# Optimization experiments

Measured on AMD Instinct MI355X. Metric: run time of the kernel, lower is better.

Reference implementation:

```python
import jax, jax.numpy as jnp
import numpy as np

DEPTH_K = 64
DEPTH_V = 64
NUM_HEADS = 8


def setup_inputs() -> dict:
    key = jax.random.key(0)
    k1, k2, k3 = jax.random.split(key, 3)
    B, H, W = 2, 48, 48
    C = 2 * DEPTH_K + DEPTH_V  # 192
    dkh = DEPTH_K // NUM_HEADS  # 8
    inputs = jax.random.normal(k1, (B, H, W, C), dtype=jnp.float32)
    # RandomNormal(stddev=dkh**-0.5) initializer
    key_rel_w = jax.random.normal(k2, (2 * W - 1, dkh), dtype=jnp.float32) * dkh ** (-0.5)
    key_rel_h = jax.random.normal(k3, (2 * H - 1, dkh), dtype=jnp.float32) * dkh ** (-0.5)
    return {"inputs": inputs, "key_rel_w": key_rel_w, "key_rel_h": key_rel_h}


def rel_to_abs(x):
    # x: [B, N, L, 2L-1] -> [B, N, L, L] via the pad/reshape skew trick
    B, N, L, _ = x.shape
    x = jnp.pad(x, ((0, 0), (0, 0), (0, 0), (0, 1)))          # [B,N,L,2L]
    flat = x.reshape(B, N, L * 2 * L)
    flat = jnp.pad(flat, ((0, 0), (0, 0), (0, L - 1)))
    final = flat.reshape(B, N, L + 1, 2 * L - 1)
    return final[:, :, :L, L - 1:]


def rel_logits_1d(q, rel_k, transpose_mask):
    # q: [B, nh, H, W, d]; rel_k: [2W-1, d]
    B, nh, H, W, d = q.shape
    rl = jnp.einsum('bhxyd,md->bhxym', q, rel_k)              # [B,nh,H,W,2W-1]
    rl = rel_to_abs(rl.reshape(B, nh * H, W, 2 * W - 1))      # [B,nh*H,W,W]
    rl = rl.reshape(B, nh, H, W, W)
    rl = jnp.broadcast_to(rl[:, :, :, None, :, :], (B, nh, H, H, W, W))
    rl = jnp.transpose(rl, transpose_mask)
    return rl.reshape(B, nh, H * W, H * W)


def attention_augmentation_2d(inputs, key_rel_w, key_rel_h):
    B, H, W, C = inputs.shape
    nh = NUM_HEADS
    dkh = DEPTH_K // nh
    dvh = DEPTH_V // nh
    q, k, v = jnp.split(inputs, [DEPTH_K, 2 * DEPTH_K], axis=-1)

    def split_heads(x):
        d = x.shape[-1] // nh
        return jnp.transpose(x.reshape(B, H, W, nh, d), (0, 3, 1, 2, 4))  # [B,nh,H,W,d]

    q = split_heads(q) * dkh ** (-0.5)
    k = split_heads(k)
    v = split_heads(v)

    flat_q = q.reshape(B, nh, H * W, dkh)
    flat_k = k.reshape(B, nh, H * W, dkh)
    flat_v = v.reshape(B, nh, H * W, dvh)

    logits = jnp.einsum('bhnd,bhmd->bhnm', flat_q, flat_k)    # [B,nh,HW,HW]
    # relative logits: width uses q as-is, height uses q with H/W swapped
    w_rel = rel_logits_1d(q, key_rel_w, (0, 1, 2, 4, 3, 5))
    h_rel = rel_logits_1d(jnp.transpose(q, (0, 1, 3, 2, 4)), key_rel_h, (0, 1, 4, 2, 5, 3))
    logits = logits + h_rel + w_rel

    weights = jax.nn.softmax(logits, axis=-1)
    attn = jnp.einsum('bhnm,bhmd->bhnd', weights, flat_v)     # [B,nh,HW,dvh]
    attn = attn.reshape(B, nh, H, W, dvh)
    out = jnp.transpose(attn, (0, 2, 3, 1, 4)).reshape(B, H, W, DEPTH_V)
    return out


def reference(inputs, key_rel_w, key_rel_h):
    return attention_augmentation_2d(inputs, key_rel_w, key_rel_h)
```

## Files before the change

### kernel.cpp

```cpp
#include <hip/hip_runtime.h>
#include <stdint.h>

#define WW 48
#define NQ 2304
#define NWT 144
#define SCL 0.51011868f
#define SHIFT 17.312340491f
#define ACCF (NWT * 2304)

typedef float v2f __attribute__((ext_vector_type(2)));

__device__ __forceinline__ v2f v2fma(v2f a, v2f b, v2f c) {
    return __builtin_elementwise_fma(a, b, c);
}

__global__ __launch_bounds__(256) void qh_pre(const float* __restrict__ in,
                                              const float* __restrict__ relh,
                                              float* __restrict__ QH) {
    const int bh = blockIdx.x / 9;
    const int nt = blockIdx.x - bh * 9;
    const int n = nt * 256 + threadIdx.x;
    const int b = bh >> 3, h = bh & 7;
    const int y = n / WW;

    const float* qp = in + ((size_t)(b * NQ + n) * 192 + h * 8);
    float4 a = *(const float4*)qp, bb = *(const float4*)(qp + 4);
    v2f Q0 = {a.x * SCL, a.y * SCL}, Q1 = {a.z * SCL, a.w * SCL};
    v2f Q2 = {bb.x * SCL, bb.y * SCL}, Q3 = {bb.z * SCL, bb.w * SCL};

    for (int y2 = 0; y2 < 48; ++y2) {
        const float* rh = relh + (y2 - y + 47) * 8;
        float4 ta = *(const float4*)rh, tb = *(const float4*)(rh + 4);
        v2f s = v2fma(Q0, (v2f){ta.x, ta.y},
                v2fma(Q1, (v2f){ta.z, ta.w},
                v2fma(Q2, (v2f){tb.x, tb.y},
                      Q3 * (v2f){tb.z, tb.w})));
        QH[(size_t)(bh * 48 + y2) * 2304 + n] = s.x + s.y - SHIFT;
    }
}

__global__ __launch_bounds__(256, 2) void attn_kernel(const float* __restrict__ in,
                                                      const float* __restrict__ relw,
                                                      const float* __restrict__ QH,
                                                      float* __restrict__ ACC) {
    __shared__ float4 lds[1152];

    const int bx = blockIdx.x;
    const int wt = bx % NWT;
    const int gg = bx / NWT;
    const int bh = wt / 9;
    const int qt = wt - bh * 9;
    const int tid = threadIdx.x;
    const int lane = tid & 63;
    const int wv = tid >> 6;
    const int kc_local = wv >> 1;
    const int rowhalf = wv & 1;
    const int kc = gg * 2 + kc_local;
    const int b = bh >> 3, h = bh & 7;

    const float4* inp4 = (const float4*)in;
    for (int t = tid; t < 1152; t += 256) {
        const int chunk = t / 576, tt = t - chunk * 576;
        const int key = tt >> 2, p = tt & 3;
        const int row = key / 3, col = key - row * 3;
        const size_t px = (size_t)(b * NQ + row * 48 + (gg * 2 + chunk) * 3 + col) * 48;
        const int c4 = (p < 2) ? (16 + h * 2 + p) : (32 + h * 2 + (p - 2));
        lds[t] = inp4[px + c4];
    }

    v2f Q0[4], Q1[4], Q2[4], Q3[4];
    int xq[4];
#pragma unroll
    for (int j = 0; j < 4; ++j) {
        const int n = qt * 256 + j * 64 + lane;
        const int y = n / WW;
        xq[j] = n - y * WW;
        const float* qp = in + ((size_t)(b * NQ + n) * 192 + h * 8);
        float4 a = *(const float4*)qp, bb = *(const float4*)(qp + 4);
        Q0[j] = (v2f){a.x * SCL, a.y * SCL};
        Q1[j] = (v2f){a.z * SCL, a.w * SCL};
        Q2[j] = (v2f){bb.x * SCL, bb.y * SCL};
        Q3[j] = (v2f){bb.z * SCL, bb.w * SCL};
    }

    float qw[4][3];
#pragma unroll
    for (int j = 0; j < 4; ++j)
#pragma unroll
        for (int c = 0; c < 3; ++c) {
            const float* rw = relw + (kc * 3 + c - xq[j] + 47) * 8;
            float4 ta = *(const float4*)rw, tb = *(const float4*)(rw + 4);
            v2f s = v2fma(Q0[j], (v2f){ta.x, ta.y},
                    v2fma(Q1[j], (v2f){ta.z, ta.w},
                    v2fma(Q2[j], (v2f){tb.x, tb.y},
                          Q3[j] * (v2f){tb.z, tb.w})));
            qw[j][c] = s.x + s.y;
        }

    __syncthreads();

    float l[4] = {0, 0, 0, 0};
    v2f A0[4], A1[4], A2[4], A3[4];
#pragma unroll
    for (int j = 0; j < 4; ++j) {
        A0[j] = (v2f){0.f, 0.f}; A1[j] = (v2f){0.f, 0.f};
        A2[j] = (v2f){0.f, 0.f}; A3[j] = (v2f){0.f, 0.f};
    }
    const float* myl = (const float*)(lds + kc_local * 576);
    const float* qhbase = QH + (size_t)bh * 48 * 2304 + qt * 256 + lane;

#pragma unroll 1
    for (int R = 0; R < 3; ++R) {
        float qh[4][8];
#pragma unroll
        for (int row = 0; row < 8; ++row) {
            const int y2 = rowhalf * 24 + R * 8 + row;
            const float* qr = qhbase + (size_t)y2 * 2304;
#pragma unroll
            for (int j = 0; j < 4; ++j) qh[j][row] = qr[j * 64];
        }

#pragma unroll 2
        for (int row = 0; row < 8; ++row) {
            const int y2 = rowhalf * 24 + R * 8 + row;
#pragma unroll
            for (int c = 0; c < 3; ++c) {
                const int base = (y2 * 3 + c) * 16;
                const float4 k0 = *(const float4*)(myl + base);
                const float4 k1 = *(const float4*)(myl + base + 4);
                const float4 v0 = *(const float4*)(myl + base + 8);
                const float4 v1 = *(const float4*)(myl + base + 12);
                const v2f K0 = {k0.x, k0.y}, K1 = {k0.z, k0.w};
                const v2f K2 = {k1.x, k1.y}, K3 = {k1.z, k1.w};
                const v2f V0 = {v0.x, v0.y}, V1 = {v0.z, v0.w};
                const v2f V2 = {v1.x, v1.y}, V3 = {v1.z, v1.w};
#pragma unroll
                for (int j = 0; j < 4; ++j) {
                    v2f d = v2fma(Q0[j], K0,
                            v2fma(Q1[j], K1,
                            v2fma(Q2[j], K2, Q3[j] * K3)));
                    const float p = __builtin_amdgcn_exp2f(
                        (qh[j][row] + qw[j][c]) + (d.x + d.y));
                    l[j] += p;
                    const v2f pp = {p, p};
                    A0[j] = v2fma(pp, V0, A0[j]);
                    A1[j] = v2fma(pp, V1, A1[j]);
                    A2[j] = v2fma(pp, V2, A2[j]);
                    A3[j] = v2fma(pp, V3, A3[j]);
                }
            }
        }
    }

    __syncthreads();
    float* mr = (float*)(lds + kc_local * 576);
    if (rowhalf == 0) {
#pragma unroll
        for (int j = 0; j < 4; ++j) {
            const int q = j * 64 + lane;
            mr[q] = l[j];
            mr[1 * 256 + q] = A0[j].x; mr[2 * 256 + q] = A0[j].y;
            mr[3 * 256 + q] = A1[j].x; mr[4 * 256 + q] = A1[j].y;
            mr[5 * 256 + q] = A2[j].x; mr[6 * 256 + q] = A2[j].y;
            mr[7 * 256 + q] = A3[j].x; mr[8 * 256 + q] = A3[j].y;
        }
    }
    __syncthreads();
    if (rowhalf == 1) {
#pragma unroll
        for (int j = 0; j < 4; ++j) {
            const int q = j * 64 + lane;
            mr[q] += l[j];
            mr[1 * 256 + q] += A0[j].x; mr[2 * 256 + q] += A0[j].y;
            mr[3 * 256 + q] += A1[j].x; mr[4 * 256 + q] += A1[j].y;
            mr[5 * 256 + q] += A2[j].x; mr[6 * 256 + q] += A2[j].y;
            mr[7 * 256 + q] += A3[j].x; mr[8 * 256 + q] += A3[j].y;
        }
    }
    __syncthreads();

    const float* r0 = (const float*)lds;
    const float* r1 = (const float*)(lds + 576);
    float* ab = ACC + (size_t)wt * 2304;
    for (int idx = tid; idx < 2304; idx += 256)
        atomicAdd(ab + idx, r0[idx] + r1[idx]);
}

__global__ __launch_bounds__(256) void norm_kernel(const float* __restrict__ ACC,
                                                   float* __restrict__ out) {
    const int t = blockIdx.x * 256 + threadIdx.x;
    const int wt = t >> 8, q = t & 255;
    const float* ab = ACC + (size_t)wt * 2304;
    const float inv = 1.0f / ab[q];
    float s[8];
#pragma unroll
    for (int e = 0; e < 8; ++e) s[e] = ab[(1 + e) * 256 + q] * inv;
    const int bh = wt / 9;
    const int qtl = wt - bh * 9;
    const int n = qtl * 256 + q;
    const int b = bh >> 3, h = bh & 7;
    float* op = out + ((size_t)(b * NQ + n) * 64 + h * 8);
    ((float4*)op)[0] = make_float4(s[0], s[1], s[2], s[3]);
    ((float4*)op)[1] = make_float4(s[4], s[5], s[6], s[7]);
}

extern "C" void kernel_launch(void* const* d_in, const int* in_sizes, int n_in,
                              void* d_out, int out_size, void* d_ws, size_t ws_size,
                              hipStream_t stream) {
    const float* in   = (const float*)d_in[0];
    const float* relw = (const float*)d_in[1];
    const float* relh = (const float*)d_in[2];
    float* ACC = (float*)d_ws;
    float* QH  = (float*)d_ws + ACCF;
    float* out = (float*)d_out;

    hipMemsetAsync(ACC, 0, ACCF * sizeof(float), stream);
    qh_pre<<<144, 256, 0, stream>>>(in, relh, QH);
    attn_kernel<<<8 * NWT, 256, 0, stream>>>(in, relw, QH, ACC);
    norm_kernel<<<144, 256, 0, stream>>>(ACC, out);
}
```

Before: 127.9 us.

## Fuse memset into qh_pre and normalization into attn via last-block counter

Zeroing of the accumulator moves into qh_pre, and the separate norm kernel is removed. Instead, the last of the 8 key-chunk blocks for each query tile, found through an atomic counter, normalizes and writes the output. The QH row loop is also restructured to load one row of QH per iteration rather than prefetching 8 rows at a time. This cuts two launches (memset and norm) at the cost of threadfences, a counter atomic per block, and possibly less latency hiding on the QH loads.

```diff
diff --git a/kernel.cpp b/kernel.cpp
--- a/kernel.cpp
+++ b/kernel.cpp
@@ -7,6 +7,7 @@
 #define SCL 0.51011868f
 #define SHIFT 17.312340491f
 #define ACCF (NWT * 2304)
+#define QHF (16 * 48 * 2304)
 
 typedef float v2f __attribute__((ext_vector_type(2)));
 
@@ -16,9 +17,16 @@
 
 __global__ __launch_bounds__(256) void qh_pre(const float* __restrict__ in,
                                               const float* __restrict__ relh,
-                                              float* __restrict__ QH) {
-    const int bh = blockIdx.x / 9;
-    const int nt = blockIdx.x - bh * 9;
+                                              float* __restrict__ QH,
+                                              float* __restrict__ ACC,
+                                              unsigned int* __restrict__ ctr) {
+    const int bx = blockIdx.x;
+    float* ab = ACC + (size_t)bx * 2304;
+    for (int i = threadIdx.x; i < 2304; i += 256) ab[i] = 0.0f;
+    if (threadIdx.x == 0) ctr[bx] = 0u;
+
+    const int bh = bx / 9;
+    const int nt = bx - bh * 9;
     const int n = nt * 256 + threadIdx.x;
     const int b = bh >> 3, h = bh & 7;
     const int y = n / WW;
@@ -42,8 +50,11 @@
 __global__ __launch_bounds__(256, 2) void attn_kernel(const float* __restrict__ in,
                                                       const float* __restrict__ relw,
                                                       const float* __restrict__ QH,
-                                                      float* __restrict__ ACC) {
+                                                      float* __restrict__ ACC,
+                                                      unsigned int* __restrict__ ctr,
+                                                      float* __restrict__ out) {
     __shared__ float4 lds[1152];
+    __shared__ int sflag;
 
     const int bx = blockIdx.x;
     const int wt = bx % NWT;
@@ -109,45 +120,38 @@
     const float* myl = (const float*)(lds + kc_local * 576);
     const float* qhbase = QH + (size_t)bh * 48 * 2304 + qt * 256 + lane;
 
-#pragma unroll 1
-    for (int R = 0; R < 3; ++R) {
-        float qh[4][8];
-#pragma unroll
-        for (int row = 0; row < 8; ++row) {
-            const int y2 = rowhalf * 24 + R * 8 + row;
-            const float* qr = qhbase + (size_t)y2 * 2304;
-#pragma unroll
-            for (int j = 0; j < 4; ++j) qh[j][row] = qr[j * 64];
-        }
-
 #pragma unroll 2
-        for (int row = 0; row < 8; ++row) {
-            const int y2 = rowhalf * 24 + R * 8 + row;
-#pragma unroll
-            for (int c = 0; c < 3; ++c) {
-                const int base = (y2 * 3 + c) * 16;
-                const float4 k0 = *(const float4*)(myl + base);
-                const float4 k1 = *(const float4*)(myl + base + 4);
-                const float4 v0 = *(const float4*)(myl + base + 8);
-                const float4 v1 = *(const float4*)(myl + base + 12);
-                const v2f K0 = {k0.x, k0.y}, K1 = {k0.z, k0.w};
-                const v2f K2 = {k1.x, k1.y}, K3 = {k1.z, k1.w};
-                const v2f V0 = {v0.x, v0.y}, V1 = {v0.z, v0.w};
-                const v2f V2 = {v1.x, v1.y}, V3 = {v1.z, v1.w};
-#pragma unroll
-                for (int j = 0; j < 4; ++j) {
-                    v2f d = v2fma(Q0[j], K0,
-                            v2fma(Q1[j], K1,
-                            v2fma(Q2[j], K2, Q3[j] * K3)));
-                    const float p = __builtin_amdgcn_exp2f(
-                        (qh[j][row] + qw[j][c]) + (d.x + d.y));
-                    l[j] += p;
-                    const v2f pp = {p, p};
-                    A0[j] = v2fma(pp, V0, A0[j]);
-                    A1[j] = v2fma(pp, V1, A1[j]);
-                    A2[j] = v2fma(pp, V2, A2[j]);
-                    A3[j] = v2fma(pp, V3, A3[j]);
-                }
+    for (int r = 0; r < 24; ++r) {
+        const int y2 = rowhalf * 24 + r;
+        const float* qr = qhbase + (size_t)y2 * 2304;
+        float qh[4];
+#pragma unroll
+        for (int j = 0; j < 4; ++j) qh[j] = qr[j * 64];
+
+#pragma unroll
+        for (int c = 0; c < 3; ++c) {
+            const int base = (y2 * 3 + c) * 16;
+            const float4 k0 = *(const float4*)(myl + base);
+            const float4 k1 = *(const float4*)(myl + base + 4);
+            const float4 v0 = *(const float4*)(myl + base + 8);
+            const float4 v1 = *(const float4*)(myl + base + 12);
+            const v2f K0 = {k0.x, k0.y}, K1 = {k0.z, k0.w};
+            const v2f K2 = {k1.x, k1.y}, K3 = {k1.z, k1.w};
+            const v2f V0 = {v0.x, v0.y}, V1 = {v0.z, v0.w};
+            const v2f V2 = {v1.x, v1.y}, V3 = {v1.z, v1.w};
+#pragma unroll
+            for (int j = 0; j < 4; ++j) {
+                v2f d = v2fma(Q0[j], K0,
+                        v2fma(Q1[j], K1,
+                        v2fma(Q2[j], K2, Q3[j] * K3)));
+                const float p = __builtin_amdgcn_exp2f(
+                    (qh[j] + qw[j][c]) + (d.x + d.y));
+                l[j] += p;
+                const v2f pp = {p, p};
+                A0[j] = v2fma(pp, V0, A0[j]);
+                A1[j] = v2fma(pp, V1, A1[j]);
+                A2[j] = v2fma(pp, V2, A2[j]);
+                A3[j] = v2fma(pp, V3, A3[j]);
             }
         }
     }
@@ -184,24 +188,27 @@
     float* ab = ACC + (size_t)wt * 2304;
     for (int idx = tid; idx < 2304; idx += 256)
         atomicAdd(ab + idx, r0[idx] + r1[idx]);
-}
-
-__global__ __launch_bounds__(256) void norm_kernel(const float* __restrict__ ACC,
-                                                   float* __restrict__ out) {
-    const int t = blockIdx.x * 256 + threadIdx.x;
-    const int wt = t >> 8, q = t & 255;
-    const float* ab = ACC + (size_t)wt * 2304;
-    const float inv = 1.0f / ab[q];
-    float s[8];
-#pragma unroll
-    for (int e = 0; e < 8; ++e) s[e] = ab[(1 + e) * 256 + q] * inv;
-    const int bh = wt / 9;
-    const int qtl = wt - bh * 9;
-    const int n = qtl * 256 + q;
-    const int b = bh >> 3, h = bh & 7;
-    float* op = out + ((size_t)(b * NQ + n) * 64 + h * 8);
-    ((float4*)op)[0] = make_float4(s[0], s[1], s[2], s[3]);
-    ((float4*)op)[1] = make_float4(s[4], s[5], s[6], s[7]);
+
+    __threadfence();
+    __syncthreads();
+    if (tid == 0) sflag = (int)atomicAdd(&ctr[wt], 1u);
+    __syncthreads();
+    if (sflag != 7) return;
+
+    __threadfence();
+    {
+        const int q = tid;
+        float s[9];
+#pragma unroll
+        for (int j = 0; j < 9; ++j)
+            s[j] = __hip_atomic_load(ab + j * 256 + q,
+                                     __ATOMIC_RELAXED, __HIP_MEMORY_SCOPE_AGENT);
+        const float inv = 1.0f / s[0];
+        const int n = qt * 256 + q;
+        float* op = out + ((size_t)(b * NQ + n) * 64 + h * 8);
+        ((float4*)op)[0] = make_float4(s[1]*inv, s[2]*inv, s[3]*inv, s[4]*inv);
+        ((float4*)op)[1] = make_float4(s[5]*inv, s[6]*inv, s[7]*inv, s[8]*inv);
+    }
 }
 
 extern "C" void kernel_launch(void* const* d_in, const int* in_sizes, int n_in,
@@ -212,10 +219,9 @@
     const float* relh = (const float*)d_in[2];
     float* ACC = (float*)d_ws;
     float* QH  = (float*)d_ws + ACCF;
+    unsigned int* ctr = (unsigned int*)((float*)d_ws + ACCF + QHF);
     float* out = (float*)d_out;
 
-    hipMemsetAsync(ACC, 0, ACCF * sizeof(float), stream);
-    qh_pre<<<144, 256, 0, stream>>>(in, relh, QH);
-    attn_kernel<<<8 * NWT, 256, 0, stream>>>(in, relw, QH, ACC);
-    norm_kernel<<<144, 256, 0, stream>>>(ACC, out);
-}
+    qh_pre<<<NWT, 256, 0, stream>>>(in, relh, QH, ACC, ctr);
+    attn_kernel<<<8 * NWT, 256, 0, stream>>>(in, relw, QH, ACC, ctr, out);
+}
```

New measurement: 187.6 us. 46.7% more time.
